# Performance work log

Hardware: AMD Instinct MI355X
Metric: run time of the kernel (lower is better)

Reference implementation:

```python
import jax, jax.numpy as jnp
import numpy as np
import math

D_MODEL = 128

def setup_inputs() -> dict:
    key = jax.random.key(0)
    k1, k2, k3, k4 = jax.random.split(key, 4)
    B, V, F = 8, 32, 512
    x = jax.random.normal(k1, (B, V, F), dtype=jnp.float32)
    # Dense(d_model) on a scalar input: kernel shape [1, d_model], no bias
    w_q = jax.random.normal(k2, (1, D_MODEL), dtype=jnp.float32)
    w_k = jax.random.normal(k3, (1, D_MODEL), dtype=jnp.float32)
    w_v = jax.random.normal(k4, (1, D_MODEL), dtype=jnp.float32)
    return {"x": x, "w_q": w_q, "w_k": w_k, "w_v": w_v}

def reference(x, w_q, w_k, w_v):
    d_model = w_q.shape[-1]
    # x: [B, V, F]; per-scalar projections -> [B, V, F, d_model]
    Q = x[..., None] * w_q[0]  # broadcast outer product
    K = x[..., None] * w_k[0]
    V = x[..., None] * w_v[0]
    # scores: [B, V, F, F]
    scores = jnp.einsum('bvfd,bvgd->bvfg', Q, K) / math.sqrt(d_model)
    attn = jax.nn.softmax(scores, axis=-1)
    attended = jnp.einsum('bvfg,bvgd->bvfd', attn, V)
    # mean over the n_filters axis -> [B, V, d_model]
    return attended.mean(axis=2)
```

## Files before the change

### kernel.cpp

```cpp
#include <hip/hip_runtime.h>
#include <math.h>


#if __has_builtin(__builtin_amdgcn_exp2f)
#define EXP2(x) __builtin_amdgcn_exp2f(x)
#else
#define EXP2(x) exp2f(x)
#endif

#define F_DIM 512
#define D_MODEL 128

__global__ __launch_bounds__(1024) void intravol_attn_kernel(
    const float* __restrict__ x,
    const float* __restrict__ wq,
    const float* __restrict__ wk,
    const float* __restrict__ wv,
    float* __restrict__ out)
{
    __shared__ float xs[F_DIM];
    __shared__ float pden[1024], pnum[1024];
    __shared__ float wmax[8], wmin[8], wsum[16];
    __shared__ float s_c, s_xmax, s_xmin;

    const int bv   = blockIdx.x;
    const int tid  = threadIdx.x;
    const int lane = tid & 63;
    const int wave = tid >> 6;

    float xv = 0.0f;
    if (tid < F_DIM) { xv = x[bv * F_DIM + tid]; xs[tid] = xv; }

    if (wave < 8) {
        float mx = xv, mn = xv;
        for (int o = 32; o > 0; o >>= 1) {
            mx = fmaxf(mx, __shfl_down(mx, o));
            mn = fminf(mn, __shfl_down(mn, o));
        }
        if (lane == 0) { wmax[wave] = mx; wmin[wave] = mn; }
    } else if (wave == 8) {
        float d = wq[lane] * wk[lane] + wq[lane + 64] * wk[lane + 64];
        for (int o = 32; o > 0; o >>= 1) d += __shfl_down(d, o);
        if (lane == 0) s_c = d * 0.08838834764831845f;
    }
    __syncthreads();
    if (tid == 0) {
        float M = wmax[0], m_ = wmin[0];
        for (int i = 1; i < 8; ++i) { M = fmaxf(M, wmax[i]); m_ = fminf(m_, wmin[i]); }
        s_xmax = M; s_xmin = m_;
    }
    __syncthreads();

    const float LOG2E = 1.4426950408889634f;
    const int   f  = tid & (F_DIM - 1);
    const int   g0 = (tid >> 9) << 8;
    const float a2 = s_c * xs[f] * LOG2E;
    const float m2 = (a2 >= 0.0f) ? a2 * s_xmax : a2 * s_xmin;

    float den = 0.0f, num = 0.0f;
    #pragma unroll 8
    for (int g = g0; g < g0 + 256; ++g) {
        const float xg = xs[g];
        const float e  = EXP2(fmaf(a2, xg, -m2));
        den += e;
        num = fmaf(e, xg, num);
    }
    pden[tid] = den; pnum[tid] = num;
    __syncthreads();

    float s_f = 0.0f;
    if (tid < F_DIM) {
        const float d = pden[tid] + pden[tid + F_DIM];
        const float n = pnum[tid] + pnum[tid + F_DIM];
        s_f = n / d;
    }
    float t = s_f;
    for (int o = 32; o > 0; o >>= 1) t += __shfl_down(t, o);
    if (lane == 0) wsum[wave] = t;
    __syncthreads();

    if (tid < D_MODEL) {
        float total = 0.0f;
        for (int i = 0; i < 16; ++i) total += wsum[i];
        out[bv * D_MODEL + tid] = total * (1.0f / (float)F_DIM) * wv[tid];
    }
}

extern "C" void kernel_launch(void* const* d_in, const int* in_sizes, int n_in,
                              void* d_out, int out_size, void* d_ws, size_t ws_size,
                              hipStream_t stream) {
    const float* x  = (const float*)d_in[0];
    const float* wq = (const float*)d_in[1];
    const float* wk = (const float*)d_in[2];
    const float* wv = (const float*)d_in[3];
    float* out = (float*)d_out;

    intravol_attn_kernel<<<256, 1024, 0, stream>>>(x, wq, wk, wv, out);
}
```

Before: 69.25 us.

## Register-tile four query rows per thread and split keys into eight slices

Each thread now handles four query positions against a 64-key slice, reading keys from shared memory as float4 and reusing each loaded key across four rows. This replaces one row against 256 keys per thread, cutting LDS reads per exp and adding independent accumulator chains for ILP. Partial sums grow to eight slices per row, so the final reduction reads eight partials per row and shared memory use rises to about 34 KB.

```diff
diff --git a/kernel.cpp b/kernel.cpp
--- a/kernel.cpp
+++ b/kernel.cpp
@@ -9,7 +9,9 @@
 #endif
 
 #define F_DIM 512
-#define D_MODEL 128
+#define NF 4
+#define NSLICE 8
+#define GS (F_DIM / NSLICE)
 
 __global__ __launch_bounds__(1024) void intravol_attn_kernel(
     const float* __restrict__ x,
@@ -18,8 +20,9 @@
     const float* __restrict__ wv,
     float* __restrict__ out)
 {
-    __shared__ float xs[F_DIM];
-    __shared__ float pden[1024], pnum[1024];
+    __shared__ __align__(16) float xs[F_DIM];
+    __shared__ __align__(16) float pden[NSLICE * F_DIM];
+    __shared__ __align__(16) float pnum[NSLICE * F_DIM];
     __shared__ float wmax[8], wmin[8], wsum[16];
     __shared__ float s_c, s_xmax, s_xmin;
 
@@ -52,26 +55,49 @@
     __syncthreads();
 
     const float LOG2E = 1.4426950408889634f;
-    const int   f  = tid & (F_DIM - 1);
-    const int   g0 = (tid >> 9) << 8;
-    const float a2 = s_c * xs[f] * LOG2E;
-    const float m2 = (a2 >= 0.0f) ? a2 * s_xmax : a2 * s_xmin;
+    const int q  = tid & 127;
+    const int sl = tid >> 7;
+    const int f0 = q << 2;
 
-    float den = 0.0f, num = 0.0f;
-    #pragma unroll 8
-    for (int g = g0; g < g0 + 256; ++g) {
-        const float xg = xs[g];
-        const float e  = EXP2(fmaf(a2, xg, -m2));
-        den += e;
-        num = fmaf(e, xg, num);
+    float a2[NF], m2n[NF], den[NF], num[NF];
+    #pragma unroll
+    for (int k = 0; k < NF; ++k) {
+        const float a = s_c * xs[f0 + k] * LOG2E;
+        a2[k]  = a;
+        m2n[k] = -((a >= 0.0f) ? a * s_xmax : a * s_xmin);
+        den[k] = 0.0f;
+        num[k] = 0.0f;
     }
-    pden[tid] = den; pnum[tid] = num;
+
+    const float4* xs4 = (const float4*)&xs[sl * GS];
+    #pragma unroll 4
+    for (int i = 0; i < GS / 4; ++i) {
+        const float4 v = xs4[i];
+        const float xg_[4] = { v.x, v.y, v.z, v.w };
+        #pragma unroll
+        for (int j = 0; j < 4; ++j) {
+            const float xg = xg_[j];
+            #pragma unroll
+            for (int k = 0; k < NF; ++k) {
+                const float e = EXP2(fmaf(a2[k], xg, m2n[k]));
+                den[k] += e;
+                num[k] = fmaf(e, xg, num[k]);
+            }
+        }
+    }
+
+    *(float4*)&pden[sl * F_DIM + f0] = make_float4(den[0], den[1], den[2], den[3]);
+    *(float4*)&pnum[sl * F_DIM + f0] = make_float4(num[0], num[1], num[2], num[3]);
     __syncthreads();
 
     float s_f = 0.0f;
     if (tid < F_DIM) {
-        const float d = pden[tid] + pden[tid + F_DIM];
-        const float n = pnum[tid] + pnum[tid + F_DIM];
+        float d = 0.0f, n = 0.0f;
+        #pragma unroll
+        for (int s2 = 0; s2 < NSLICE; ++s2) {
+            d += pden[s2 * F_DIM + tid];
+            n += pnum[s2 * F_DIM + tid];
+        }
         s_f = n / d;
     }
     float t = s_f;
@@ -79,10 +105,11 @@
     if (lane == 0) wsum[wave] = t;
     __syncthreads();
 
-    if (tid < D_MODEL) {
+    if (tid < 128) {
         float total = 0.0f;
+        #pragma unroll
         for (int i = 0; i < 16; ++i) total += wsum[i];
-        out[bv * D_MODEL + tid] = total * (1.0f / (float)F_DIM) * wv[tid];
+        out[bv * 128 + tid] = total * (1.0f / (float)F_DIM) * wv[tid];
     }
 }
 
```

After: 67.45 us. -2.6%, faster.

## Split each row across four blocks, register-tile two queries per thread

Applied to the files above, without the earlier changes.

The single kernel (256 blocks of 1024 threads) becomes two kernels. The first launches 1024 blocks of 512 threads, each handling 128 query positions of one row. Every thread computes two queries over 64 keys, reading keys as float4 from shared memory and writing a partial sum to a workspace. A second small kernel adds the four partials per row and scales by wv. This spreads work over more CUs and reuses each loaded key for two queries, at the cost of a second launch, a global-memory round trip, and each block redoing the row load and max/min reduction.

```diff
diff --git a/kernel.cpp b/kernel.cpp
--- a/kernel.cpp
+++ b/kernel.cpp
@@ -9,81 +9,98 @@
 #endif
 
 #define F_DIM 512
-#define D_MODEL 128
 
-__global__ __launch_bounds__(1024) void intravol_attn_kernel(
+__global__ __launch_bounds__(512) void intravol_p1(
     const float* __restrict__ x,
     const float* __restrict__ wq,
     const float* __restrict__ wk,
-    const float* __restrict__ wv,
-    float* __restrict__ out)
+    float* __restrict__ part)
 {
-    __shared__ float xs[F_DIM];
-    __shared__ float pden[1024], pnum[1024];
-    __shared__ float wmax[8], wmin[8], wsum[16];
+    __shared__ __align__(16) float xs[F_DIM];
+    __shared__ float pden[8][128];
+    __shared__ float pnum[8][128];
+    __shared__ float wmax[8], wmin[8], wsum[2];
     __shared__ float s_c, s_xmax, s_xmin;
 
-    const int bv   = blockIdx.x;
     const int tid  = threadIdx.x;
     const int lane = tid & 63;
     const int wave = tid >> 6;
+    const int row  = blockIdx.x >> 2;
+    const int prt  = blockIdx.x & 3;
 
-    float xv = 0.0f;
-    if (tid < F_DIM) { xv = x[bv * F_DIM + tid]; xs[tid] = xv; }
-
-    if (wave < 8) {
-        float mx = xv, mn = xv;
-        for (int o = 32; o > 0; o >>= 1) {
-            mx = fmaxf(mx, __shfl_down(mx, o));
-            mn = fminf(mn, __shfl_down(mn, o));
-        }
-        if (lane == 0) { wmax[wave] = mx; wmin[wave] = mn; }
-    } else if (wave == 8) {
+    const float xv = x[row * F_DIM + tid];
+    xs[tid] = xv;
+    float mx = xv, mn = xv;
+    for (int o = 32; o > 0; o >>= 1) {
+        mx = fmaxf(mx, __shfl_down(mx, o));
+        mn = fminf(mn, __shfl_down(mn, o));
+    }
+    if (lane == 0) { wmax[wave] = mx; wmin[wave] = mn; }
+    __syncthreads();
+    if (tid == 0) {
+        float M = wmax[0], m_ = wmin[0];
+        #pragma unroll
+        for (int i = 1; i < 8; ++i) { M = fmaxf(M, wmax[i]); m_ = fminf(m_, wmin[i]); }
+        s_xmax = M; s_xmin = m_;
+    } else if (wave == 1) {
         float d = wq[lane] * wk[lane] + wq[lane + 64] * wk[lane + 64];
         for (int o = 32; o > 0; o >>= 1) d += __shfl_down(d, o);
         if (lane == 0) s_c = d * 0.08838834764831845f;
     }
     __syncthreads();
-    if (tid == 0) {
-        float M = wmax[0], m_ = wmin[0];
-        for (int i = 1; i < 8; ++i) { M = fmaxf(M, wmax[i]); m_ = fminf(m_, wmin[i]); }
-        s_xmax = M; s_xmin = m_;
+
+    const float LOG2E = 1.4426950408889634f;
+    const int sl = tid >> 6;
+    const int fl = (tid & 63) << 1;
+    const int f  = (prt << 7) + fl;
+
+    const float a0 = s_c * xs[f]     * LOG2E;
+    const float a1 = s_c * xs[f + 1] * LOG2E;
+    const float b0 = -((a0 >= 0.0f) ? a0 * s_xmax : a0 * s_xmin);
+    const float b1 = -((a1 >= 0.0f) ? a1 * s_xmax : a1 * s_xmin);
+
+    float d0 = 0.0f, d1 = 0.0f, n0 = 0.0f, n1 = 0.0f;
+    const float4* xs4 = (const float4*)&xs[sl << 6];
+    #pragma unroll
+    for (int i = 0; i < 16; ++i) {
+        const float4 v = xs4[i];
+        const float xg_[4] = { v.x, v.y, v.z, v.w };
+        #pragma unroll
+        for (int j = 0; j < 4; ++j) {
+            const float xg = xg_[j];
+            const float e0 = EXP2(fmaf(a0, xg, b0));
+            const float e1 = EXP2(fmaf(a1, xg, b1));
+            d0 += e0; n0 = fmaf(e0, xg, n0);
+            d1 += e1; n1 = fmaf(e1, xg, n1);
+        }
     }
+    pden[sl][fl] = d0; pden[sl][fl + 1] = d1;
+    pnum[sl][fl] = n0; pnum[sl][fl + 1] = n1;
     __syncthreads();
 
-    const float LOG2E = 1.4426950408889634f;
-    const int   f  = tid & (F_DIM - 1);
-    const int   g0 = (tid >> 9) << 8;
-    const float a2 = s_c * xs[f] * LOG2E;
-    const float m2 = (a2 >= 0.0f) ? a2 * s_xmax : a2 * s_xmin;
+    float sf = 0.0f;
+    if (tid < 128) {
+        float D = 0.0f, N = 0.0f;
+        #pragma unroll
+        for (int s = 0; s < 8; ++s) { D += pden[s][tid]; N += pnum[s][tid]; }
+        sf = N / D;
+    }
+    float t = sf;
+    for (int o = 32; o > 0; o >>= 1) t += __shfl_down(t, o);
+    if (lane == 0 && wave < 2) wsum[wave] = t;
+    __syncthreads();
+    if (tid == 0) part[blockIdx.x] = wsum[0] + wsum[1];
+}
 
-    float den = 0.0f, num = 0.0f;
-    #pragma unroll 8
-    for (int g = g0; g < g0 + 256; ++g) {
-        const float xg = xs[g];
-        const float e  = EXP2(fmaf(a2, xg, -m2));
-        den += e;
-        num = fmaf(e, xg, num);
-    }
-    pden[tid] = den; pnum[tid] = num;
-    __syncthreads();
-
-    float s_f = 0.0f;
-    if (tid < F_DIM) {
-        const float d = pden[tid] + pden[tid + F_DIM];
-        const float n = pnum[tid] + pnum[tid + F_DIM];
-        s_f = n / d;
-    }
-    float t = s_f;
-    for (int o = 32; o > 0; o >>= 1) t += __shfl_down(t, o);
-    if (lane == 0) wsum[wave] = t;
-    __syncthreads();
-
-    if (tid < D_MODEL) {
-        float total = 0.0f;
-        for (int i = 0; i < 16; ++i) total += wsum[i];
-        out[bv * D_MODEL + tid] = total * (1.0f / (float)F_DIM) * wv[tid];
-    }
+__global__ __launch_bounds__(128) void intravol_p2(
+    const float* __restrict__ part,
+    const float* __restrict__ wv,
+    float* __restrict__ out)
+{
+    const int r = blockIdx.x;
+    const int t = threadIdx.x;
+    const float S = part[4 * r] + part[4 * r + 1] + part[4 * r + 2] + part[4 * r + 3];
+    out[r * 128 + t] = S * (1.0f / (float)F_DIM) * wv[t];
 }
 
 extern "C" void kernel_launch(void* const* d_in, const int* in_sizes, int n_in,
@@ -93,7 +110,9 @@
     const float* wq = (const float*)d_in[1];
     const float* wk = (const float*)d_in[2];
     const float* wv = (const float*)d_in[3];
-    float* out = (float*)d_out;
+    float* out  = (float*)d_out;
+    float* part = (float*)d_ws;
 
-    intravol_attn_kernel<<<256, 1024, 0, stream>>>(x, wq, wk, wv, out);
+    intravol_p1<<<1024, 512, 0, stream>>>(x, wq, wk, part);
+    intravol_p2<<<256, 128, 0, stream>>>(part, wv, out);
 }
```

Measured after the change: 69.79 us. About the same (+0.8%).

## Process two query rows per thread with packed float2 math and float4 key loads

Applied to the files above, without the earlier changes.

Each thread now handles two query positions f over a quarter of the keys, where it used to handle one query over half of them. Key values come from shared memory as float4 and are reused across both queries, and the fma and accumulate steps use two-wide vectors so the compiler can emit packed FP32 instructions. This cuts LDS traffic per exp. The cost is more registers and a four-way partial reduction through shared memory.

```diff
diff --git a/kernel.cpp b/kernel.cpp
--- a/kernel.cpp
+++ b/kernel.cpp
@@ -8,29 +8,30 @@
 #define EXP2(x) exp2f(x)
 #endif
 
+typedef float v2f __attribute__((ext_vector_type(2)));
+
 #define F_DIM 512
-#define D_MODEL 128
 
-__global__ __launch_bounds__(1024) void intravol_attn_kernel(
+__global__ __launch_bounds__(1024) void intravol_attn(
     const float* __restrict__ x,
     const float* __restrict__ wq,
     const float* __restrict__ wk,
     const float* __restrict__ wv,
     float* __restrict__ out)
 {
-    __shared__ float xs[F_DIM];
-    __shared__ float pden[1024], pnum[1024];
-    __shared__ float wmax[8], wmin[8], wsum[16];
+    __shared__ __align__(16) float xs[F_DIM];
+    __shared__ __align__(8) float pden[4][F_DIM];
+    __shared__ __align__(8) float pnum[4][F_DIM];
+    __shared__ float wmax[8], wmin[8], wsum[8];
     __shared__ float s_c, s_xmax, s_xmin;
 
-    const int bv   = blockIdx.x;
     const int tid  = threadIdx.x;
     const int lane = tid & 63;
     const int wave = tid >> 6;
+    const int row  = blockIdx.x;
 
     float xv = 0.0f;
-    if (tid < F_DIM) { xv = x[bv * F_DIM + tid]; xs[tid] = xv; }
-
+    if (tid < F_DIM) { xv = x[row * F_DIM + tid]; xs[tid] = xv; }
     if (wave < 8) {
         float mx = xv, mn = xv;
         for (int o = 32; o > 0; o >>= 1) {
@@ -46,43 +47,60 @@
     __syncthreads();
     if (tid == 0) {
         float M = wmax[0], m_ = wmin[0];
+        #pragma unroll
         for (int i = 1; i < 8; ++i) { M = fmaxf(M, wmax[i]); m_ = fminf(m_, wmin[i]); }
         s_xmax = M; s_xmin = m_;
     }
     __syncthreads();
 
     const float LOG2E = 1.4426950408889634f;
-    const int   f  = tid & (F_DIM - 1);
-    const int   g0 = (tid >> 9) << 8;
-    const float a2 = s_c * xs[f] * LOG2E;
-    const float m2 = (a2 >= 0.0f) ? a2 * s_xmax : a2 * s_xmin;
+    const int f0 = (tid & 255) << 1;
+    const int sl = tid >> 8;
 
-    float den = 0.0f, num = 0.0f;
+    const float a0 = s_c * xs[f0]     * LOG2E;
+    const float a1 = s_c * xs[f0 + 1] * LOG2E;
+    v2f a2  = { a0, a1 };
+    v2f bb  = { -((a0 >= 0.0f) ? a0 * s_xmax : a0 * s_xmin),
+                -((a1 >= 0.0f) ? a1 * s_xmax : a1 * s_xmin) };
+    v2f den = { 0.0f, 0.0f };
+    v2f num = { 0.0f, 0.0f };
+
+    const float4* xs4 = (const float4*)&xs[sl << 7];
     #pragma unroll 8
-    for (int g = g0; g < g0 + 256; ++g) {
-        const float xg = xs[g];
-        const float e  = EXP2(fmaf(a2, xg, -m2));
-        den += e;
-        num = fmaf(e, xg, num);
+    for (int i = 0; i < 32; ++i) {
+        const float4 v = xs4[i];
+        const float xg_[4] = { v.x, v.y, v.z, v.w };
+        #pragma unroll
+        for (int j = 0; j < 4; ++j) {
+            const float xg = xg_[j];
+            const v2f xg2 = { xg, xg };
+            const v2f arg = __builtin_elementwise_fma(a2, xg2, bb);
+            const v2f e   = { EXP2(arg.x), EXP2(arg.y) };
+            den += e;
+            num = __builtin_elementwise_fma(e, xg2, num);
+        }
     }
-    pden[tid] = den; pnum[tid] = num;
+    *(v2f*)&pden[sl][f0] = den;
+    *(v2f*)&pnum[sl][f0] = num;
     __syncthreads();
 
-    float s_f = 0.0f;
+    float sf = 0.0f;
     if (tid < F_DIM) {
-        const float d = pden[tid] + pden[tid + F_DIM];
-        const float n = pnum[tid] + pnum[tid + F_DIM];
-        s_f = n / d;
+        float D = 0.0f, N = 0.0f;
+        #pragma unroll
+        for (int s = 0; s < 4; ++s) { D += pden[s][tid]; N += pnum[s][tid]; }
+        sf = N / D;
     }
-    float t = s_f;
+    float t = sf;
     for (int o = 32; o > 0; o >>= 1) t += __shfl_down(t, o);
-    if (lane == 0) wsum[wave] = t;
+    if (lane == 0 && wave < 8) wsum[wave] = t;
     __syncthreads();
 
-    if (tid < D_MODEL) {
+    if (tid < 128) {
         float total = 0.0f;
-        for (int i = 0; i < 16; ++i) total += wsum[i];
-        out[bv * D_MODEL + tid] = total * (1.0f / (float)F_DIM) * wv[tid];
+        #pragma unroll
+        for (int i = 0; i < 8; ++i) total += wsum[i];
+        out[row * 128 + tid] = total * (1.0f / (float)F_DIM) * wv[tid];
     }
 }
 
@@ -95,5 +113,5 @@
     const float* wv = (const float*)d_in[3];
     float* out = (float*)d_out;
 
-    intravol_attn_kernel<<<256, 1024, 0, stream>>>(x, wq, wk, wv, out);
+    intravol_attn<<<256, 1024, 0, stream>>>(x, wq, wk, wv, out);
 }
```

Result: faster. 66.61 us (-3.8%).
